# Kernel optimization log

Measured on AMD Instinct MI355X. Metric: run time of the kernel, lower is better.

The kernel has to match this reference:

```python
import jax, jax.numpy as jnp
import numpy as np
import math

# Fixed rendering constants (from module-level source)
FOV_X = 60.0
FOV_Y = 60.0
NEAR = 0.1
FAR = 10000.0
SCALE_MODIFIER = 1.0
MAX_FREQUENCY = 128.0
NUM_TOTAL_FREQUENCIES = 1024
GAUSSIAN_ONLY = False
COV_DILATION = 0.3  # low-pass dilation as in 3DGS EWA splatting

N_PRIM = 512
TOP_K = 8
IMG_H = 200
IMG_W = 200


def _quat_to_rotmat(q):
    # q: [N,4] (r, x, y, z), normalized
    q = q / (jnp.linalg.norm(q, axis=-1, keepdims=True) + 1e-8)
    r, x, y, z = q[:, 0], q[:, 1], q[:, 2], q[:, 3]
    R = jnp.stack([
        jnp.stack([1 - 2 * (y * y + z * z), 2 * (x * y - r * z), 2 * (x * z + r * y)], -1),
        jnp.stack([2 * (x * y + r * z), 1 - 2 * (x * x + z * z), 2 * (y * z - r * x)], -1),
        jnp.stack([2 * (x * z - r * y), 2 * (y * z + r * x), 1 - 2 * (x * x + y * y)], -1),
    ], axis=-2)  # [N,3,3]
    return R


def _forward(colors, opacities, background_color, positions, scales, rotations,
             topk_wave_coefficients, topk_wave_indices, cam_position,
             view_matrix, VP_matrix, image_width, image_height):
    H, W = image_height, image_width
    N = positions.shape[0]
    tan_x = math.tan(math.radians(FOV_X * 0.5))
    tan_y = math.tan(math.radians(FOV_Y * 0.5))
    fx = W / (2.0 * tan_x)
    fy = H / (2.0 * tan_y)

    # --- 3D covariance: Sigma = R diag(s^2) R^T, s = exp(log_scales) * modifier
    R = _quat_to_rotmat(rotations)                     # [N,3,3]
    s = jnp.exp(scales) * SCALE_MODIFIER               # [N,3]
    Sigma = jnp.einsum('nij,nj,nkj->nik', R, s * s, R)  # [N,3,3]

    # --- projection
    p_hom = jnp.concatenate([positions, jnp.ones((N, 1), positions.dtype)], -1)  # [N,4]
    t_cam = jnp.einsum('ij,nj->ni', view_matrix, p_hom)[:, :3]                   # [N,3] camera space
    clip = jnp.einsum('ij,nj->ni', VP_matrix, p_hom)                             # [N,4]
    wclip = clip[:, 3:4]
    ndc = clip[:, :2] / jnp.where(jnp.abs(wclip) > 1e-6, wclip, 1e-6)
    px = (ndc * 0.5 + 0.5) * jnp.array([W, H], positions.dtype)                  # [N,2] pixel center
    depth = t_cam[:, 2]

    # --- EWA 2D covariance: cov2d = J Wr Sigma Wr^T J^T + dilation
    tz = jnp.maximum(depth, NEAR)
    tx, ty = t_cam[:, 0], t_cam[:, 1]
    zeros = jnp.zeros_like(tz)
    J = jnp.stack([
        jnp.stack([fx / tz, zeros, -fx * tx / (tz * tz)], -1),
        jnp.stack([zeros, fy / tz, -fy * ty / (tz * tz)], -1),
    ], axis=-2)                                         # [N,2,3]
    Wr = view_matrix[:3, :3]
    M = jnp.einsum('nij,jk->nik', J, Wr)                # [N,2,3]
    cov2d = jnp.einsum('nab,nbc,ndc->nad', M, Sigma, M) # [N,2,2]
    A = cov2d[:, 0, 0] + COV_DILATION
    B = cov2d[:, 0, 1]
    C = cov2d[:, 1, 1] + COV_DILATION
    det = jnp.maximum(A * C - B * B, 1e-12)
    conA, conB, conC = C / det, -B / det, A / det       # conic (inverse cov)

    # --- pixel grid [H*W]
    ys = jnp.arange(H, dtype=positions.dtype) + 0.5
    xs = jnp.arange(W, dtype=positions.dtype) + 0.5
    gy, gx = jnp.meshgrid(ys, xs, indexing='ij')
    gx, gy = gx.ravel(), gy.ravel()

    dx = px[:, 0:1] - gx[None, :]                       # [N,HW]
    dy = px[:, 1:2] - gy[None, :]
    power = -0.5 * (conA[:, None] * dx * dx + conC[:, None] * dy * dy) - conB[:, None] * dx * dy
    G = jnp.exp(jnp.minimum(power, 0.0))                # [N,HW]

    # --- periodic (Gabor) modulation along projected primary axis of each primitive
    if GAUSSIAN_ONLY:
        wave = 1.0
    else:
        a3 = R[:, :, 0]                                  # local first axis, world space [N,3]
        a2 = jnp.einsum('nij,nj->ni', M, a3)             # projected to screen [N,2]
        a2 = a2 / (jnp.linalg.norm(a2, axis=-1, keepdims=True) + 1e-8)
        tcoord = (dx * a2[:, 0:1] + dy * a2[:, 1:2]) / W  # [N,HW], normalized coord
        freqs = topk_wave_indices.astype(positions.dtype) * (MAX_FREQUENCY / NUM_TOTAL_FREQUENCIES)  # [N,K]
        wave = jnp.zeros_like(tcoord)
        for k in range(topk_wave_indices.shape[1]):      # small fixed K, unrolled
            wave = wave + topk_wave_coefficients[:, k:k + 1] * jnp.cos(
                2.0 * jnp.pi * freqs[:, k:k + 1] * tcoord)

    alpha = jnp.clip(opacities * G * wave, 0.0, 0.99)   # [N,HW]
    valid = (depth > NEAR) & (wclip[:, 0] > 1e-4)
    alpha = jnp.where(valid[:, None], alpha, 0.0)

    # --- depth sort + front-to-back alpha compositing
    order = jnp.argsort(depth)
    alpha_s = alpha[order]
    colors_s = colors[order]
    Tprod = jnp.cumprod(1.0 - alpha_s, axis=0)           # inclusive transmittance
    T_excl = jnp.concatenate([jnp.ones((1, alpha_s.shape[1]), alpha_s.dtype), Tprod[:-1]], 0)
    img = jnp.einsum('nc,np->cp', colors_s, alpha_s * T_excl)  # [3,HW]
    img = img + background_color[:, None] * Tprod[-1][None, :]
    return img.reshape(3, H, W)


def setup_inputs() -> dict:
    key = jax.random.key(0)
    ks = jax.random.split(key, 10)
    N, K = N_PRIM, TOP_K
    colors = jax.random.uniform(ks[0], (N, 3), jnp.float32)
    opacities = 0.8 * jax.random.uniform(ks[1], (N, 1), jnp.float32)
    background_color = jnp.zeros((3,), jnp.float32)
    # positions inside the view frustum: z in [4,12], xy in [-3,3]
    xy = jax.random.uniform(ks[2], (N, 2), jnp.float32, -3.0, 3.0)
    z = jax.random.uniform(ks[3], (N, 1), jnp.float32, 4.0, 12.0)
    positions = jnp.concatenate([xy, z], -1)
    scales = -2.5 + 0.3 * jax.random.normal(ks[4], (N, 3), jnp.float32)  # log-scales
    rotations = jax.random.normal(ks[5], (N, 4), jnp.float32)
    topk_wave_coefficients = 0.1 * jax.random.normal(ks[6], (N, K), jnp.float32)
    topk_wave_indices = jax.random.randint(ks[7], (N, K), 1, NUM_TOTAL_FREQUENCIES).astype(jnp.int32)
    cam_position = jnp.zeros((3,), jnp.float32)
    view_matrix = jnp.eye(4, dtype=jnp.float32)
    tan_x = math.tan(math.radians(FOV_X * 0.5))
    tan_y = math.tan(math.radians(FOV_Y * 0.5))
    P = jnp.array([[1.0 / tan_x, 0, 0, 0],
                   [0, 1.0 / tan_y, 0, 0],
                   [0, 0, FAR / (FAR - NEAR), -FAR * NEAR / (FAR - NEAR)],
                   [0, 0, 1.0, 0]], jnp.float32)
    VP_matrix = P @ view_matrix
    return {
        'colors': colors, 'opacities': opacities, 'background_color': background_color,
        'positions': positions, 'scales': scales, 'rotations': rotations,
        'topk_wave_coefficients': topk_wave_coefficients, 'topk_wave_indices': topk_wave_indices,
        'cam_position': cam_position, 'view_matrix': view_matrix, 'VP_matrix': VP_matrix,
        'image_width': IMG_W, 'image_height': IMG_H,
    }


def reference(colors, opacities, background_color, positions, scales, rotations,
              topk_wave_coefficients, topk_wave_indices, cam_position,
              view_matrix, VP_matrix, image_width, image_height):
    return _forward(colors, opacities, background_color, positions, scales, rotations,
                    topk_wave_coefficients, topk_wave_indices, cam_position,
                    view_matrix, VP_matrix, image_width, image_height)
```

## Files before the change

kernel.cpp:

```cpp
#include <hip/hip_runtime.h>
#include <math.h>

#define NPRIM   512
#define TOPK    8
#define PSTRIDE 28
#define IMG     200
#define NPIX    (IMG * IMG)
#define NSEG    8
#define SEGSZ   (NPRIM / NSEG)
#define TILE    64
#define TILES_X (IMG / 8)
#define NTILES  (TILES_X * TILES_X)
#define GRID    209


__global__ __launch_bounds__(NPRIM) void fused_kernel(
    const float* __restrict__ colors,
    const float* __restrict__ opacities,
    const float* __restrict__ positions,
    const float* __restrict__ scales,
    const float* __restrict__ rotations,
    const float* __restrict__ wcoef,
    const int*   __restrict__ widx,
    const float* __restrict__ view,
    const float* __restrict__ VP,
    const float* __restrict__ bg,
    float* __restrict__ out)
{
    __shared__ float  lds[NPRIM * PSTRIDE];
    __shared__ float4 sbb[NPRIM];
    __shared__ float4 part[NSEG * TILE];
    __shared__ float  sd[NPRIM];

    const int n = threadIdx.x;

    {
        const float tanx = 0.57735026918962576451f;
        const float fx = IMG / (2.0f * tanx);
        const float fy = IMG / (2.0f * tanx);

        float qr = rotations[n*4+0], qx = rotations[n*4+1];
        float qy = rotations[n*4+2], qz = rotations[n*4+3];
        float qn = sqrtf(qr*qr + qx*qx + qy*qy + qz*qz) + 1e-8f;
        qr /= qn; qx /= qn; qy /= qn; qz /= qn;
        float R00 = 1.f - 2.f*(qy*qy + qz*qz), R01 = 2.f*(qx*qy - qr*qz), R02 = 2.f*(qx*qz + qr*qy);
        float R10 = 2.f*(qx*qy + qr*qz), R11 = 1.f - 2.f*(qx*qx + qz*qz), R12 = 2.f*(qy*qz - qr*qx);
        float R20 = 2.f*(qx*qz - qr*qy), R21 = 2.f*(qy*qz + qr*qx), R22 = 1.f - 2.f*(qx*qx + qy*qy);

        float s0 = expf(scales[n*3+0]); s0 *= s0;
        float s1 = expf(scales[n*3+1]); s1 *= s1;
        float s2 = expf(scales[n*3+2]); s2 *= s2;

        float S00 = R00*R00*s0 + R01*R01*s1 + R02*R02*s2;
        float S01 = R00*R10*s0 + R01*R11*s1 + R02*R12*s2;
        float S02 = R00*R20*s0 + R01*R21*s1 + R02*R22*s2;
        float S11 = R10*R10*s0 + R11*R11*s1 + R12*R12*s2;
        float S12 = R10*R20*s0 + R11*R21*s1 + R12*R22*s2;
        float S22 = R20*R20*s0 + R21*R21*s1 + R22*R22*s2;

        float px_ = positions[n*3+0], py_ = positions[n*3+1], pz_ = positions[n*3+2];
        float t0 = view[0]*px_ + view[1]*py_ + view[2]*pz_  + view[3];
        float t1 = view[4]*px_ + view[5]*py_ + view[6]*pz_  + view[7];
        float t2 = view[8]*px_ + view[9]*py_ + view[10]*pz_ + view[11];
        float c0 = VP[0]*px_  + VP[1]*py_  + VP[2]*pz_  + VP[3];
        float c1 = VP[4]*px_  + VP[5]*py_  + VP[6]*pz_  + VP[7];
        float w  = VP[12]*px_ + VP[13]*py_ + VP[14]*pz_ + VP[15];

        float denom = (fabsf(w) > 1e-6f) ? w : 1e-6f;
        float pxs = (c0/denom * 0.5f + 0.5f) * (float)IMG;
        float pys = (c1/denom * 0.5f + 0.5f) * (float)IMG;

        float depth = t2;
        float tz = fmaxf(depth, 0.1f);
        float invz = 1.f / tz;
        float J00 = fx*invz, J02 = -fx*t0*invz*invz;
        float J11 = fy*invz, J12 = -fy*t1*invz*invz;

        float M00 = J00*view[0] + J02*view[8];
        float M01 = J00*view[1] + J02*view[9];
        float M02 = J00*view[2] + J02*view[10];
        float M10 = J11*view[4] + J12*view[8];
        float M11 = J11*view[5] + J12*view[9];
        float M12 = J11*view[6] + J12*view[10];

        float T00 = M00*S00 + M01*S01 + M02*S02;
        float T01 = M00*S01 + M01*S11 + M02*S12;
        float T02 = M00*S02 + M01*S12 + M02*S22;
        float T10 = M10*S00 + M11*S01 + M12*S02;
        float T11 = M10*S01 + M11*S11 + M12*S12;
        float T12 = M10*S02 + M11*S12 + M12*S22;
        float cA = T00*M00 + T01*M01 + T02*M02 + 0.3f;
        float cB = T00*M10 + T01*M11 + T02*M12;
        float cC = T10*M10 + T11*M11 + T12*M12 + 0.3f;
        float det  = fmaxf(cA*cC - cB*cB, 1e-12f);
        float idet = 1.f / det;
        float conA = cC*idet, conB = -cB*idet, conC = cA*idet;

        float a2x = M00*R00 + M01*R10 + M02*R20;
        float a2y = M10*R00 + M11*R10 + M12*R20;
        float an = sqrtf(a2x*a2x + a2y*a2y) + 1e-8f;
        a2x = (a2x/an) * (1.0f/(float)IMG);
        a2y = (a2y/an) * (1.0f/(float)IMG);

        bool valid = (depth > 0.1f) && (w > 1e-4f);
        float op = valid ? opacities[n] : 0.0f;

        float rx = valid ? sqrtf(fmaxf(30.f * cA, 0.f)) : -1e30f;
        float ry = valid ? sqrtf(fmaxf(30.f * cC, 0.f)) : -1e30f;

        sd[n] = depth;
        __syncthreads();
        int rank = 0;
#pragma unroll 8
        for (int m = 0; m < NPRIM; ++m) {
            float dm = sd[m];
            rank += (dm < depth) || (dm == depth && m < n);
        }

        float* e = lds + rank * PSTRIDE;
        e[0]=pxs; e[1]=pys; e[2]=conA; e[3]=conB; e[4]=conC;
        e[5]=a2x; e[6]=a2y; e[7]=op;
        e[8]=colors[n*3+0]; e[9]=colors[n*3+1]; e[10]=colors[n*3+2]; e[11]=0.f;
#pragma unroll
        for (int k = 0; k < TOPK; ++k) {
            e[12+k] = wcoef[n*TOPK+k];
            e[20+k] = 0.78539816339744830962f * (float)widx[n*TOPK+k];
        }
        sbb[rank] = make_float4(pxs, pys, rx, ry);
    }
    __syncthreads();

    const int lane = n & 63;
    const int wv   = n >> 6;
    const float4 bb = sbb[wv * SEGSZ + lane];
    const float* seg = lds + (wv * SEGSZ) * PSTRIDE;
    const float bg0 = bg[0], bg1 = bg[1], bg2 = bg[2];

    for (int t = blockIdx.x; t < NTILES; t += GRID) {
        const int tx = t % TILES_X, ty = t / TILES_X;
        const int x  = tx*8 + (lane & 7);
        const int y  = ty*8 + (lane >> 3);
        const float gx = (float)x + 0.5f, gy = (float)y + 0.5f;

        const float tcx = (float)(tx*8) + 4.0f, tcy = (float)(ty*8) + 4.0f;
        bool active = (fabsf(bb.x - tcx) <= bb.z + 3.5f) &&
                      (fabsf(bb.y - tcy) <= bb.w + 3.5f);
        unsigned long long mask = __ballot(active);

        float T = 1.f, cr = 0.f, cg = 0.f, cb = 0.f;
        while (mask) {
            int j = __ffsll((unsigned long long)mask) - 1;
            mask &= mask - 1;
            const float* h = seg + j * PSTRIDE;
            float4 q0 = *(const float4*)(h);
            float4 q1 = *(const float4*)(h + 4);
            float dx = q0.x - gx, dy = q0.y - gy;
            float pw = -0.5f*(q0.z*dx*dx + q1.x*dy*dy) - q0.w*dx*dy;
            if (__any(pw > -15.0f)) {
                float4 q2 = *(const float4*)(h + 8);
                float4 c0 = *(const float4*)(h + 12), c1 = *(const float4*)(h + 16);
                float4 w0 = *(const float4*)(h + 20), w1 = *(const float4*)(h + 24);
                float G = __expf(fminf(pw, 0.f));
                float tt = dx*q1.y + dy*q1.z;
                float wave = c0.x*__cosf(w0.x*tt) + c0.y*__cosf(w0.y*tt)
                           + c0.z*__cosf(w0.z*tt) + c0.w*__cosf(w0.w*tt)
                           + c1.x*__cosf(w1.x*tt) + c1.y*__cosf(w1.y*tt)
                           + c1.z*__cosf(w1.z*tt) + c1.w*__cosf(w1.w*tt);
                float a = fminf(fmaxf(q1.w * G * wave, 0.f), 0.99f);
                float wgt = a * T;
                cr += q2.x*wgt; cg += q2.y*wgt; cb += q2.z*wgt;
                T *= (1.f - a);
            }
        }
        part[wv*TILE + lane] = make_float4(cr, cg, cb, T);

        __syncthreads();

        if (n < TILE) {
            float Ta = 1.f, fr = 0.f, fg = 0.f, fb = 0.f;
#pragma unroll
            for (int s = 0; s < NSEG; ++s) {
                float4 v = part[s*TILE + lane];
                fr += Ta * v.x; fg += Ta * v.y; fb += Ta * v.z;
                Ta *= v.w;
            }
            const int p = y*IMG + x;
            out[p]          = fr + bg0*Ta;
            out[NPIX + p]   = fg + bg1*Ta;
            out[2*NPIX + p] = fb + bg2*Ta;
        }
        __syncthreads();
    }
}

extern "C" void kernel_launch(void* const* d_in, const int* in_sizes, int n_in,
                              void* d_out, int out_size, void* d_ws, size_t ws_size,
                              hipStream_t stream) {
    const float* colors  = (const float*)d_in[0];
    const float* opac    = (const float*)d_in[1];
    const float* bg      = (const float*)d_in[2];
    const float* pos     = (const float*)d_in[3];
    const float* scales  = (const float*)d_in[4];
    const float* rot     = (const float*)d_in[5];
    const float* wcoef   = (const float*)d_in[6];
    const int*   widx    = (const int*)d_in[7];
    const float* view    = (const float*)d_in[9];
    const float* VP      = (const float*)d_in[10];

    hipLaunchKernelGGL(fused_kernel, dim3(GRID), dim3(NPRIM), 0, stream,
                       colors, opac, pos, scales, rot, wcoef, widx, view, VP,
                       bg, (float*)d_out);
}
```

Measured before the change: 98.78 us.

## Replace O(N^2) rank-counting depth sort with bitonic sort network

Each thread previously computed its depth rank by scanning all 512 depths in shared memory. It now builds a 64-bit key from the sign-flipped depth bits and the primitive index, and runs a bitonic sort. Warp shuffles handle strides under 64 and shared memory with barriers handles larger strides. An inverse permutation written to shared memory then gives each thread its rank. This cuts per-thread sort work from 512 compares to about 45 stages, at the cost of many block-wide barriers during the preamble that every block repeats.

Measured after the change: 90.06 us. 8.8% less time.

```diff
diff --git a/kernel.cpp b/kernel.cpp
--- a/kernel.cpp
+++ b/kernel.cpp
@@ -30,7 +30,7 @@
     __shared__ float  lds[NPRIM * PSTRIDE];
     __shared__ float4 sbb[NPRIM];
     __shared__ float4 part[NSEG * TILE];
-    __shared__ float  sd[NPRIM];
+    __shared__ unsigned long long sk[NPRIM];
 
     const int n = threadIdx.x;
 
@@ -108,14 +108,34 @@
         float rx = valid ? sqrtf(fmaxf(30.f * cA, 0.f)) : -1e30f;
         float ry = valid ? sqrtf(fmaxf(30.f * cC, 0.f)) : -1e30f;
 
-        sd[n] = depth;
-        __syncthreads();
-        int rank = 0;
-#pragma unroll 8
-        for (int m = 0; m < NPRIM; ++m) {
-            float dm = sd[m];
-            rank += (dm < depth) || (dm == depth && m < n);
-        }
+        unsigned db = __float_as_uint(depth);
+        db = (db & 0x80000000u) ? ~db : (db | 0x80000000u);
+        unsigned long long kreg = ((unsigned long long)db << 32) | (unsigned)n;
+
+#pragma unroll
+        for (int k = 2; k <= NPRIM; k <<= 1) {
+#pragma unroll
+            for (int j = k >> 1; j > 0; j >>= 1) {
+                unsigned long long vp;
+                if (j >= 64) {
+                    sk[n] = kreg;
+                    __syncthreads();
+                    vp = sk[n ^ j];
+                    __syncthreads();
+                } else {
+                    vp = __shfl_xor(kreg, j, 64);
+                }
+                bool takeMin = (((n & k) == 0) == ((n & j) == 0));
+                unsigned long long mn = (kreg < vp) ? kreg : vp;
+                unsigned long long mx = (kreg < vp) ? vp : kreg;
+                kreg = takeMin ? mn : mx;
+            }
+        }
+        __syncthreads();
+        int* sinv = (int*)sk;
+        sinv[(unsigned)kreg] = n;
+        __syncthreads();
+        int rank = sinv[n];
 
         float* e = lds + rank * PSTRIDE;
         e[0]=pxs; e[1]=pys; e[2]=conA; e[3]=conB; e[4]=conC;
@@ -206,6 +226,7 @@
     const int*   widx    = (const int*)d_in[7];
     const float* view    = (const float*)d_in[9];
     const float* VP      = (const float*)d_in[10];
+    (void)d_ws; (void)ws_size;
 
     hipLaunchKernelGGL(fused_kernel, dim3(GRID), dim3(NPRIM), 0, stream,
                        colors, opac, pos, scales, rot, wcoef, widx, view, VP,
```
